# Optimization experiments

Hardware: AMD Instinct MI355X
Metric: run time of the kernel (lower is better)

The kernel has to match this reference:

```python
import jax, jax.numpy as jnp
import numpy as np

BN_EPS = 1e-5
STRIDE = 8  # encoder output stride -> upsample target is H*8


def conv2d(x, w, pad):
    return jax.lax.conv_general_dilated(
        x, w, (1, 1), [(pad, pad), (pad, pad)],
        dimension_numbers=('NCHW', 'OIHW', 'NCHW'))


def batchnorm(x, gamma, beta):
    # training-mode BN (batch statistics), matching a freshly-constructed torch module
    m = jnp.mean(x, axis=(0, 2, 3), keepdims=True)
    v = jnp.var(x, axis=(0, 2, 3), keepdims=True)
    xn = (x - m) * jax.lax.rsqrt(v + BN_EPS)
    return xn * gamma[None, :, None, None] + beta[None, :, None, None]


def setup_inputs() -> dict:
    key = jax.random.key(0)
    ks = jax.random.split(key, 8)
    B, C, H, W = 8, 256, 60, 60
    NC = 2
    return {
        'V_a': jax.random.normal(ks[0], (B, C, H, W), jnp.float32),
        'V_b': jax.random.normal(ks[1], (B, C, H, W), jnp.float32),
        'W_sim': jax.random.normal(ks[2], (C, C), jnp.float32) * 0.02,
        'gate_w': jax.random.normal(ks[3], (1, C, 1, 1), jnp.float32) * 0.01,
        'convA_w': jax.random.normal(ks[4], (C, 2 * C, 3, 3), jnp.float32) * 0.01,
        'convB_w': jax.random.normal(ks[5], (C, 2 * C, 3, 3), jnp.float32) * 0.01,
        'bnA_gamma': jnp.ones((C,), jnp.float32),
        'bnA_beta': jnp.zeros((C,), jnp.float32),
        'bnB_gamma': jnp.ones((C,), jnp.float32),
        'bnB_beta': jnp.zeros((C,), jnp.float32),
        'clsA_w': jax.random.normal(ks[6], (NC, C, 1, 1), jnp.float32) * 0.01,
        'clsA_b': jnp.zeros((NC,), jnp.float32),
        'clsB_w': jax.random.normal(ks[7], (NC, C, 1, 1), jnp.float32) * 0.01,
        'clsB_b': jnp.zeros((NC,), jnp.float32),
    }


def reference(V_a, V_b, W_sim, gate_w, convA_w, convB_w,
              bnA_gamma, bnA_beta, bnB_gamma, bnB_beta,
              clsA_w, clsA_b, clsB_w, clsB_b):
    B, C, H, W = V_a.shape
    HW = H * W
    out_h, out_w = H * STRIDE, W * STRIDE

    Va = V_a.reshape(B, C, HW)  # [B,C,HW_a]
    Vb = V_b.reshape(B, C, HW)  # [B,C,HW_b]

    # Linear on V_a^T: out[b,i,d] = sum_c Va[b,c,i] * W_sim[d,c]
    WVa = jnp.einsum('dc,bci->bdi', W_sim, Va)           # [B,C,HW_a]
    S = jnp.einsum('bdi,bdj->bij', WVa, Vb)              # [B,HW_a,HW_b]

    S_row = jax.nn.softmax(S, axis=1)                    # softmax over a-positions
    A_col = jax.nn.softmax(S, axis=2)                    # softmax over b-positions

    Z_b = jnp.einsum('bci,bij->bcj', Va, S_row).reshape(B, C, H, W)
    Z_a = jnp.einsum('bcj,bij->bci', Vb, A_col).reshape(B, C, H, W)

    mask_a = jax.nn.sigmoid(conv2d(Z_a, gate_w, 0))
    mask_b = jax.lax.stop_gradient(jax.nn.sigmoid(conv2d(Z_b, gate_w, 0)))
    Z_a = Z_a * mask_a
    Z_b = Z_b * mask_b

    Z_a = jnp.concatenate([Z_a, V_a], axis=1)            # [B,2C,H,W]
    Z_b = jnp.concatenate([Z_b, V_b], axis=1)

    Z_a = jax.nn.relu(batchnorm(conv2d(Z_a, convA_w, 1), bnA_gamma, bnA_beta))
    Z_b = jax.nn.relu(batchnorm(conv2d(Z_b, convB_w, 1), bnB_gamma, bnB_beta))

    x1 = conv2d(Z_a, clsA_w, 0) + clsA_b[None, :, None, None]
    x2 = conv2d(Z_b, clsB_w, 0) + clsB_b[None, :, None, None]

    NC = x1.shape[1]
    x1 = jax.image.resize(x1, (B, NC, out_h, out_w), method='bilinear')
    x2 = jax.image.resize(x2, (B, NC, out_h, out_w), method='bilinear')

    return jnp.stack([jax.nn.sigmoid(x1), jax.nn.sigmoid(x2)])  # [2,B,NC,out_h,out_w]
```

## Files before the change

### kernel.cpp

```cpp
#include <hip/hip_runtime.h>

#define C_CH   256
#define BATCH  8
#define HW     3600
#define CHW    (C_CH*HW)
#define NPIX   (BATCH*HW)
#define KCONV  4608
#define OHW    480
#define KP     3648
#define NROWP  3712
#define XPIX   3844
#define NT     57

typedef __attribute__((ext_vector_type(8))) short s16x8;
typedef __attribute__((ext_vector_type(4))) float f32x4;

__device__ __forceinline__ unsigned short f2bf(float f){
  unsigned int u = __float_as_uint(f);
  u += 0x7FFF + ((u>>16)&1);
  return (unsigned short)(u>>16);
}

__device__ __forceinline__ void gload16(const void* g, void* l){
  __builtin_amdgcn_global_load_lds((const __attribute__((address_space(1))) void*)g,
                                   (__attribute__((address_space(3))) void*)l, 16, 0, 0);
}

__device__ __forceinline__ void gemm_core(const char* a0, const char* b0,
                                          size_t lda, size_t ldb, int nkt,
                                          f32x4 acc[4][4]){
  __shared__ __align__(16) char LDS[32768];
  const int tid = threadIdx.x, l = tid & 63, w = tid >> 6;
  char* AsW = LDS + w*1024;
  char* BsW = LDS + 16384 + w*1024;
  const int arow = (w>>1)*64 + (l&15);
  const int brow = (w&1)*64 + (l&15);
  const int kc0 = (((l>>4)*16)      ) ^ ((l&7)<<4);
  const int kc1 = (((l>>4)*16) + 64 ) ^ ((l&7)<<4);
  const char* Ab = LDS;
  const char* Bb = LDS + 16384;
  for (int kt = 0; kt < nkt; ++kt){
#pragma unroll
    for (int i=0;i<4;i++){
      gload16(a0 + (size_t)(i*32)*lda + (size_t)kt*128, AsW + i*4096);
      gload16(b0 + (size_t)(i*32)*ldb + (size_t)kt*128, BsW + i*4096);
    }
    asm volatile("s_waitcnt vmcnt(0)" ::: "memory");
    __syncthreads();
    s16x8 af[4][2], bf[4][2];
#pragma unroll
    for (int f=0;f<4;f++){
      af[f][0] = *(const s16x8*)(Ab + (arow+f*16)*128 + kc0);
      af[f][1] = *(const s16x8*)(Ab + (arow+f*16)*128 + kc1);
      bf[f][0] = *(const s16x8*)(Bb + (brow+f*16)*128 + kc0);
      bf[f][1] = *(const s16x8*)(Bb + (brow+f*16)*128 + kc1);
    }
#pragma unroll
    for (int ks=0;ks<2;ks++)
#pragma unroll
      for (int fm=0;fm<4;fm++)
#pragma unroll
        for (int fn=0;fn<4;fn++)
          acc[fm][fn] = __builtin_amdgcn_mfma_f32_16x16x32_bf16(af[fm][ks], bf[fn][ks], acc[fm][fn], 0,0,0);
    __syncthreads();
  }
}

__global__ __launch_bounds__(256) void k_gemm_wva(const unsigned short* __restrict__ VaT,
                                                  const unsigned short* __restrict__ Wsim16,
                                                  unsigned short* __restrict__ WVaT){
  const int tid = threadIdx.x, l = tid&63, w = tid>>6;
  const int b = blockIdx.z;
  const int n0 = blockIdx.x*128, m0 = blockIdx.y*128;
  const int colS = ((tid&7)*16) ^ (((tid>>3)&7)<<4);
  const char* a0 = (const char*)(VaT + (size_t)b*NROWP*256) + (size_t)(m0 + (tid>>3))*512 + colS;
  const char* b0 = (const char*)Wsim16 + (size_t)(n0 + (tid>>3))*512 + colS;
  f32x4 acc[4][4] = {};
  gemm_core(a0, b0, 512, 512, 4, acc);
  unsigned short* ob = WVaT + (size_t)b*NROWP*256;
  const int mb = m0 + (w>>1)*64 + (l>>4)*4;
  const int nb = n0 + (w&1)*64 + (l&15);
#pragma unroll
  for (int fm=0;fm<4;fm++)
#pragma unroll
    for (int fn=0;fn<4;fn++){
      int n = nb + fn*16;
#pragma unroll
      for (int r=0;r<4;r++){
        int m = mb + fm*16 + r;
        if (m < HW) ob[(size_t)m*256 + n] = f2bf(acc[fm][fn][r]);
      }
    }
}

__global__ __launch_bounds__(256) void flash_attn(const char* __restrict__ WVaT,
                                                  const char* __restrict__ VbT,
                                                  const char* __restrict__ VaT,
                                                  const char* __restrict__ Va16,
                                                  const char* __restrict__ Vb16,
                                                  const float* __restrict__ gw,
                                                  unsigned short* __restrict__ XtA,
                                                  unsigned short* __restrict__ XtB){
  __shared__ __align__(16) char LDS[73728];
  const int tid = threadIdx.x, l = tid&63, w = tid>>6;
  const int b = blockIdx.y, side = blockIdx.z;
  const size_t tOff = (size_t)b*NROWP*512;
  const size_t vOff = (size_t)b*256*KP*2;
  const char* QT = (side ? VbT  : WVaT) + tOff;
  const char* Kt = (side ? WVaT : VbT ) + tOff;
  const char* Vp = (side ? Va16 : Vb16) + vOff;
  const char* Vc = (side ? VbT  : VaT ) + tOff;
  unsigned short* Xt = (side ? XtB : XtA) + (size_t)b*XPIX*512;
  const int i0 = blockIdx.x*64;

  char* Kls = LDS;
  char* Vls = LDS + 32768;
  char* Pls = LDS + 65536;

  s16x8 q[8];
  {
    const char* qp = QT + (size_t)(i0 + w*16 + (l&15))*512 + (l>>4)*16;
#pragma unroll
    for (int ks=0;ks<8;ks++) q[ks] = *(const s16x8*)(qp + ks*64);
  }
  float gwv[4];
#pragma unroll
  for (int fn=0;fn<4;fn++) gwv[fn] = gw[w*64 + fn*16 + (l&15)];

  f32x4 acc[4][4] = {};
  f32x4 lac = {0.f,0.f,0.f,0.f};

  auto stageK = [&](int t){
    const char* src = Kt + (size_t)t*32768;
#pragma unroll
    for (int p=0;p<8;p++){
      int row = p*8 + (tid>>5), ch = tid&31;
      gload16(src + (size_t)row*512 + ((ch*16) ^ ((row&7)<<4)), Kls + p*4096 + tid*16);
    }
  };
  auto stageV = [&](int t){
#pragma unroll
    for (int p=0;p<8;p++){
      int row = p*32 + (tid>>3), ch = tid&7;
      gload16(Vp + (size_t)row*(KP*2) + (size_t)t*128 + ((ch*16) ^ ((row&7)<<4)),
              Vls + p*4096 + tid*16);
    }
  };

  stageK(0); stageV(0);
  asm volatile("s_waitcnt vmcnt(0)" ::: "memory");
  __syncthreads();

  for (int t=0; t<NT; ++t){
    f32x4 sac[4] = {};
#pragma unroll
    for (int ks=0;ks<8;ks++){
      s16x8 bk[4];
#pragma unroll
      for (int fn=0;fn<4;fn++){
        int row = fn*16 + (l&15);
        bk[fn] = *(const s16x8*)(Kls + row*512 + ((ks*64 + (l>>4)*16) ^ ((row&7)<<4)));
      }
#pragma unroll
      for (int fn=0;fn<4;fn++)
        sac[fn] = __builtin_amdgcn_mfma_f32_16x16x32_bf16(q[ks], bk[fn], sac[fn], 0,0,0);
    }
    const int j0 = t*64;
#pragma unroll
    for (int fn=0;fn<4;fn++){
      int col = fn*16 + (l&15);
      bool jv = (j0 + col) < HW;
#pragma unroll
      for (int r=0;r<4;r++){
        float e = jv ? __expf(sac[fn][r]) : 0.f;
        lac[r] += e;
        int row = w*16 + (l>>4)*4 + r;
        *(unsigned short*)(Pls + row*128 + ((col*2) ^ ((row&7)<<4))) = f2bf(e);
      }
    }
    __syncthreads();
    if (t+1 < NT) stageK(t+1);
#pragma unroll
    for (int ks=0;ks<2;ks++){
      s16x8 ap[4], bv[4];
#pragma unroll
      for (int fm=0;fm<4;fm++){
        int row = fm*16 + (l&15);
        ap[fm] = *(const s16x8*)(Pls + row*128 + ((ks*64 + (l>>4)*16) ^ ((row&7)<<4)));
      }
#pragma unroll
      for (int fn=0;fn<4;fn++){
        int row = w*64 + fn*16 + (l&15);
        bv[fn] = *(const s16x8*)(Vls + row*128 + ((ks*64 + (l>>4)*16) ^ ((row&7)<<4)));
      }
#pragma unroll
      for (int fm=0;fm<4;fm++)
#pragma unroll
        for (int fn=0;fn<4;fn++)
          acc[fm][fn] = __builtin_amdgcn_mfma_f32_16x16x32_bf16(ap[fm], bv[fn], acc[fm][fn], 0,0,0);
    }
    __syncthreads();
    if (t+1 < NT){
      stageV(t+1);
      asm volatile("s_waitcnt vmcnt(0)" ::: "memory");
    }
    __syncthreads();
  }

  float* Lred = (float*)(LDS + 65536);
  float* Mls  = Lred + 64;
  float* Gp   = Mls + 64;
#pragma unroll
  for (int r=0;r<4;r++){
    float v = lac[r];
    v += __shfl_xor(v,1); v += __shfl_xor(v,2); v += __shfl_xor(v,4); v += __shfl_xor(v,8);
    if ((l&15)==0) Lred[w*16 + (l>>4)*4 + r] = 1.f / v;
  }
  __syncthreads();
#pragma unroll
  for (int fm=0;fm<4;fm++){
#pragma unroll
    for (int r=0;r<4;r++){
      float v = acc[fm][0][r]*gwv[0] + acc[fm][1][r]*gwv[1]
              + acc[fm][2][r]*gwv[2] + acc[fm][3][r]*gwv[3];
      v += __shfl_xor(v,1); v += __shfl_xor(v,2); v += __shfl_xor(v,4); v += __shfl_xor(v,8);
      if ((l&15)==0) Gp[w*64 + fm*16 + (l>>4)*4 + r] = v;
    }
  }
  __syncthreads();
  if (tid < 64){
    float g = (Gp[tid] + Gp[64+tid] + Gp[128+tid] + Gp[192+tid]) * Lred[tid];
    Mls[tid] = 1.f/(1.f + __expf(-g));
  }
  __syncthreads();
  char* Ost = LDS;
#pragma unroll
  for (int fm=0;fm<4;fm++){
    float4 li = *(const float4*)&Lred[fm*16 + (l>>4)*4];
    float4 mk = *(const float4*)&Mls [fm*16 + (l>>4)*4];
    float s0 = li.x*mk.x, s1 = li.y*mk.y, s2 = li.z*mk.z, s3 = li.w*mk.w;
#pragma unroll
    for (int fn=0;fn<4;fn++){
      int col = w*64 + fn*16 + (l&15);
      int row = fm*16 + (l>>4)*4;
      *(unsigned short*)(Ost + (row+0)*512 + col*2) = f2bf(acc[fm][fn][0]*s0);
      *(unsigned short*)(Ost + (row+1)*512 + col*2) = f2bf(acc[fm][fn][1]*s1);
      *(unsigned short*)(Ost + (row+2)*512 + col*2) = f2bf(acc[fm][fn][2]*s2);
      *(unsigned short*)(Ost + (row+3)*512 + col*2) = f2bf(acc[fm][fn][3]*s3);
    }
  }
  __syncthreads();
  {
    int row = tid>>2, ch = tid&3;
    int p = i0 + row;
    if (p < HW){
      int y = p/60, x = p - y*60;
      char* dst = (char*)Xt + (size_t)((y+1)*62 + (x+1))*1024 + ch*128;
      const char* osrc = Ost + row*512 + ch*128;
      const char* vsrc = Vc + (size_t)p*512 + ch*128;
#pragma unroll
      for (int q8=0;q8<8;q8++) *(uint4*)(dst + q8*16) = *(const uint4*)(osrc + q8*16);
#pragma unroll
      for (int q8=0;q8<8;q8++) *(uint4*)(dst + 512 + q8*16) = *(const uint4*)(vsrc + q8*16);
    }
  }
}

__global__ __launch_bounds__(256) void k_gemm_conv(const unsigned short* __restrict__ WcA,
                                                   const unsigned short* __restrict__ WcB,
                                                   const unsigned short* __restrict__ XtA,
                                                   const unsigned short* __restrict__ XtB,
                                                   float* __restrict__ Ra, float* __restrict__ Rb){
  __shared__ __align__(16) char LDS[32768];
  const int tid = threadIdx.x, l = tid&63, w = tid>>6;
  const unsigned short* Wc = blockIdx.z ? WcB : WcA;
  const unsigned short* Xt = blockIdx.z ? XtB : XtA;
  float* R = blockIdx.z ? Rb : Ra;
  const int n0 = blockIdx.x*128, m0 = blockIdx.y*128;
  const int colS = ((tid&7)*16) ^ (((tid>>3)&7)<<4);
  const int srow = tid>>3;
  const char* a0 = (const char*)Wc + (size_t)(m0+srow)*(KCONV*2) + colS;
  size_t bbase[4];
#pragma unroll
  for (int i=0;i<4;i++){
    int n = n0 + i*32 + srow;
    int bb = n/HW, p = n - bb*HW;
    int y = p/60, x = p - y*60;
    bbase[i] = ((size_t)bb*XPIX + (size_t)(y+1)*62 + (x+1))*1024 + colS;
  }
  char* AsW = LDS + w*1024;
  char* BsW = LDS + 16384 + w*1024;
  const int arow = (w>>1)*64 + (l&15);
  const int brow = (w&1)*64 + (l&15);
  const int kc0 = (((l>>4)*16)      ) ^ ((l&7)<<4);
  const int kc1 = (((l>>4)*16) + 64 ) ^ ((l&7)<<4);
  const char* Ab = LDS;
  const char* Bb = LDS + 16384;
  f32x4 acc[4][4] = {};
  for (int kt = 0; kt < 72; ++kt){
    const int sh = kt>>3;
    const int ci0b = (kt&7)*128;
    const int dy = sh/3 - 1, dx = (sh - (sh/3)*3) - 1;
    const int boff = (dy*62 + dx)*1024 + ci0b;
#pragma unroll
    for (int i=0;i<4;i++){
      gload16(a0 + (size_t)(i*32)*(KCONV*2) + (size_t)kt*128, AsW + i*4096);
      gload16((const char*)Xt + bbase[i] + boff, BsW + i*4096);
    }
    asm volatile("s_waitcnt vmcnt(0)" ::: "memory");
    __syncthreads();
    s16x8 af[4][2], bfr[4][2];
#pragma unroll
    for (int f=0;f<4;f++){
      af[f][0]  = *(const s16x8*)(Ab + (arow+f*16)*128 + kc0);
      af[f][1]  = *(const s16x8*)(Ab + (arow+f*16)*128 + kc1);
      bfr[f][0] = *(const s16x8*)(Bb + (brow+f*16)*128 + kc0);
      bfr[f][1] = *(const s16x8*)(Bb + (brow+f*16)*128 + kc1);
    }
#pragma unroll
    for (int ks=0;ks<2;ks++)
#pragma unroll
      for (int fm=0;fm<4;fm++)
#pragma unroll
        for (int fn=0;fn<4;fn++)
          acc[fm][fn] = __builtin_amdgcn_mfma_f32_16x16x32_bf16(af[fm][ks], bfr[fn][ks], acc[fm][fn], 0,0,0);
    __syncthreads();
  }
  const int mb = m0 + (w>>1)*64 + (l>>4)*4;
  const int nb = n0 + (w&1)*64 + (l&15);
#pragma unroll
  for (int fm=0;fm<4;fm++)
#pragma unroll
    for (int fn=0;fn<4;fn++){
      int n = nb + fn*16;
      int bb = n/HW, p = n - bb*HW;
      float* op = R + (size_t)bb*CHW + (size_t)(mb+fm*16)*HW + p;
#pragma unroll
      for (int r=0;r<4;r++) op[(size_t)r*HW] = acc[fm][fn][r];
    }
}

__global__ __launch_bounds__(256) void zerok(uint4* __restrict__ p, int n){
  int i = blockIdx.x*256 + threadIdx.x;
  if (i < n) p[i] = make_uint4(0,0,0,0);
}

__global__ __launch_bounds__(256) void convert_bf16(const float* __restrict__ in, unsigned short* __restrict__ out, int n){
  int i = blockIdx.x*256 + threadIdx.x;
  if (i < n) out[i] = f2bf(in[i]);
}

__global__ __launch_bounds__(256) void convw(const float* __restrict__ in, unsigned short* __restrict__ out){
  int idx = blockIdx.x*256 + threadIdx.x;
  int co = idx / KCONV;
  int kp = idx - co*KCONV;
  int sh = kp >> 9, ci = kp & 511;
  out[idx] = f2bf(in[co*KCONV + ci*9 + sh]);
}

__global__ __launch_bounds__(256) void convv(const float* __restrict__ in, unsigned short* __restrict__ out){
  int idx = blockIdx.x*256 + threadIdx.x;
  int row = idx / KP;
  int k = idx - row*KP;
  out[idx] = (k < HW) ? f2bf(in[(size_t)row*HW + k]) : 0;
}

__global__ __launch_bounds__(256) void convt(const float* __restrict__ in, unsigned short* __restrict__ out){
  __shared__ unsigned short T[64][66];
  const int b = blockIdx.y;
  const int i0 = blockIdx.x*64;
  const float* inb = in + (size_t)b*CHW;
  unsigned short* ob = out + (size_t)b*NROWP*256;
  for (int cc=0; cc<4; ++cc){
    __syncthreads();
    int i = i0 + (threadIdx.x & 63);
    int ic = i < HW ? i : HW-1;
#pragma unroll
    for (int r=0;r<16;r++){
      int cl = (threadIdx.x>>6)*16 + r;
      T[cl][threadIdx.x & 63] = f2bf(inb[(size_t)(cc*64+cl)*HW + ic]);
    }
    __syncthreads();
    int il = threadIdx.x>>2, seg = threadIdx.x&3;
    unsigned short tmp[16];
#pragma unroll
    for (int e=0;e<16;e++) tmp[e] = T[seg*16+e][il];
    *(s16x8*)(ob + (size_t)(i0+il)*256 + cc*64 + seg*16)     = *(const s16x8*)tmp;
    *(s16x8*)(ob + (size_t)(i0+il)*256 + cc*64 + seg*16 + 8) = *(const s16x8*)(tmp+8);
  }
}

__global__ __launch_bounds__(256) void bn_stats(const float* __restrict__ X, float* __restrict__ sums){
  int co = blockIdx.x;
  float s = 0.f, ss = 0.f;
  for (int i = threadIdx.x; i < NPIX; i += 256){
    int bi = i / HW, p = i - bi*HW;
    float v = X[(size_t)bi*CHW + (size_t)co*HW + p];
    s += v; ss += v*v;
  }
  __shared__ float rs[256], rss[256];
  rs[threadIdx.x] = s; rss[threadIdx.x] = ss; __syncthreads();
  for (int off=128; off>0; off>>=1){
    if (threadIdx.x < off){ rs[threadIdx.x] += rs[threadIdx.x+off]; rss[threadIdx.x] += rss[threadIdx.x+off]; }
    __syncthreads();
  }
  if (threadIdx.x==0){ sums[co] = rs[0]; sums[256+co] = rss[0]; }
}

__global__ __launch_bounds__(256) void cls_kernel(const float* __restrict__ R, const float* __restrict__ sums,
                                                  const float* __restrict__ gamma, const float* __restrict__ beta,
                                                  const float* __restrict__ cw, const float* __restrict__ cb,
                                                  float* __restrict__ Xout){
  __shared__ float red[2][4][64];
  int tx = threadIdx.x & 63, ty = threadIdx.x >> 6;
  int n = blockIdx.x*64 + tx;
  int bi = n / HW, p = n - bi*HW;
  float a0 = 0.f, a1 = 0.f;
  const float invN = 1.f/28800.f;
  for (int c = ty*64; c < ty*64+64; ++c){
    float mean = sums[c]*invN;
    float var  = sums[256+c]*invN - mean*mean;
    float sc   = gamma[c]*rsqrtf(var + 1e-5f);
    float shv  = beta[c] - mean*sc;
    float v = R[(size_t)bi*CHW + (size_t)c*HW + p]*sc + shv;
    v = fmaxf(v, 0.f);
    a0 += v*cw[c]; a1 += v*cw[256+c];
  }
  red[0][ty][tx] = a0; red[1][ty][tx] = a1; __syncthreads();
  if (ty==0){
    float r0 = red[0][0][tx]+red[0][1][tx]+red[0][2][tx]+red[0][3][tx] + cb[0];
    float r1 = red[1][0][tx]+red[1][1][tx]+red[1][2][tx]+red[1][3][tx] + cb[1];
    Xout[((size_t)bi*2 + 0)*HW + p] = r0;
    Xout[((size_t)bi*2 + 1)*HW + p] = r1;
  }
}

__global__ __launch_bounds__(256) void resize_kernel(const float* __restrict__ X1, const float* __restrict__ X2,
                                                     float* __restrict__ Out){
  int idx = blockIdx.x*256 + threadIdx.x;
  int ox = idx % OHW; int t = idx / OHW;
  int oy = t % OHW;  t /= OHW;
  int nc = t & 1;    t >>= 1;
  int bi = t & 7;    int s = t >> 3;
  const float* X = (s == 0) ? X1 : X2;
  float fy = (oy + 0.5f)*0.125f - 0.5f;
  float fx = (ox + 0.5f)*0.125f - 0.5f;
  float y0f = floorf(fy), x0f = floorf(fx);
  float wy = fy - y0f, wx = fx - x0f;
  int y0 = (int)y0f, x0 = (int)x0f;
  int y1 = min(max(y0+1,0),59), x1 = min(max(x0+1,0),59);
  y0 = min(max(y0,0),59); x0 = min(max(x0,0),59);
  const float* Xp = X + ((size_t)bi*2 + nc)*HW;
  float v00 = Xp[y0*60+x0], v01 = Xp[y0*60+x1];
  float v10 = Xp[y1*60+x0], v11 = Xp[y1*60+x1];
  float v = v00*(1.f-wy)*(1.f-wx) + v01*(1.f-wy)*wx + v10*wy*(1.f-wx) + v11*wy*wx;
  Out[idx] = 1.f/(1.f+__expf(-v));
}

extern "C" void kernel_launch(void* const* d_in, const int* in_sizes, int n_in,
                              void* d_out, int out_size, void* d_ws, size_t ws_size,
                              hipStream_t stream){
  const float* Va    = (const float*)d_in[0];
  const float* Vb    = (const float*)d_in[1];
  const float* Wsim  = (const float*)d_in[2];
  const float* gw    = (const float*)d_in[3];
  const float* cwA   = (const float*)d_in[4];
  const float* cwB   = (const float*)d_in[5];
  const float* gA    = (const float*)d_in[6];
  const float* bA    = (const float*)d_in[7];
  const float* gB    = (const float*)d_in[8];
  const float* bB    = (const float*)d_in[9];
  const float* clsAw = (const float*)d_in[10];
  const float* clsAb = (const float*)d_in[11];
  const float* clsBw = (const float*)d_in[12];
  const float* clsBb = (const float*)d_in[13];
  float* out = (float*)d_out;

  char* wsb = (char*)d_ws;
  size_t off = 0;
  auto alloc = [&](size_t bytes)->void*{
    void* pt = wsb + off;
    off += (bytes + 255) & ~(size_t)255;
    return pt;
  };
  unsigned short* Va16   = (unsigned short*)alloc((size_t)8*256*KP*2);
  unsigned short* Vb16   = (unsigned short*)alloc((size_t)8*256*KP*2);
  unsigned short* VaT16  = (unsigned short*)alloc((size_t)8*NROWP*256*2);
  unsigned short* VbT16  = (unsigned short*)alloc((size_t)8*NROWP*256*2);
  unsigned short* WVaT16 = (unsigned short*)alloc((size_t)8*NROWP*256*2);
  unsigned short* Wsim16 = (unsigned short*)alloc((size_t)256*256*2);
  unsigned short* WcA16  = (unsigned short*)alloc((size_t)256*KCONV*2);
  unsigned short* WcB16  = (unsigned short*)alloc((size_t)256*KCONV*2);
  unsigned short* XtA    = (unsigned short*)alloc((size_t)8*XPIX*512*2);
  unsigned short* XtB    = (unsigned short*)alloc((size_t)8*XPIX*512*2);
  float* sumsA= (float*)alloc(512*4);
  float* sumsB= (float*)alloc(512*4);
  float* Ra = (float*)Va16;
  float* Rb = (float*)VaT16;
  float* x1 = (float*)WVaT16;
  float* x2 = x1 + (size_t)BATCH*2*HW;

  zerok<<<dim3(15376), dim3(256), 0, stream>>>((uint4*)XtA, 3936256);
  convert_bf16<<<dim3(256), dim3(256), 0, stream>>>(Wsim, Wsim16, 65536);
  convw<<<dim3(4608), dim3(256), 0, stream>>>(cwA, WcA16);
  convw<<<dim3(4608), dim3(256), 0, stream>>>(cwB, WcB16);
  convv<<<dim3(29184), dim3(256), 0, stream>>>(Va, Va16);
  convv<<<dim3(29184), dim3(256), 0, stream>>>(Vb, Vb16);
  convt<<<dim3(57,8), dim3(256), 0, stream>>>(Va, VaT16);
  convt<<<dim3(57,8), dim3(256), 0, stream>>>(Vb, VbT16);
  k_gemm_wva<<<dim3(2,29,8), dim3(256), 0, stream>>>(VaT16, Wsim16, WVaT16);

  flash_attn<<<dim3(57,8,2), dim3(256), 0, stream>>>(
      (const char*)WVaT16, (const char*)VbT16, (const char*)VaT16,
      (const char*)Va16, (const char*)Vb16, gw, XtA, XtB);

  k_gemm_conv<<<dim3(225,2,2), dim3(256), 0, stream>>>(WcA16, WcB16, XtA, XtB, Ra, Rb);
  bn_stats<<<dim3(256), dim3(256), 0, stream>>>(Ra, sumsA);
  bn_stats<<<dim3(256), dim3(256), 0, stream>>>(Rb, sumsB);
  cls_kernel<<<dim3(450), dim3(256), 0, stream>>>(Ra, sumsA, gA, bA, clsAw, clsAb, x1);
  cls_kernel<<<dim3(450), dim3(256), 0, stream>>>(Rb, sumsB, gB, bB, clsBw, clsBb, x2);
  resize_kernel<<<dim3(28800), dim3(256), 0, stream>>>(x1, x2, out);
}
```

Measured before the change: 852.8 us.

## Load V tiles directly into registers and shrink LDS for higher occupancy

Removes the LDS staging buffer for the V operand in the flash attention kernel, so each wave loads its V fragments straight from global memory into registers at the top of each tile iteration. This cuts LDS from 72KB to 40KB, drops one pair of barriers per iteration, and adds a launch-bounds hint for three blocks per CU. The P-tile swizzle changes to match the new layout. In exchange, V reads are uncoalesced per-lane 16-byte global loads with higher latency exposure, and there is extra register pressure from holding bv.

```diff
diff --git a/kernel.cpp b/kernel.cpp
--- a/kernel.cpp
+++ b/kernel.cpp
@@ -93,7 +93,7 @@
     }
 }
 
-__global__ __launch_bounds__(256) void flash_attn(const char* __restrict__ WVaT,
+__global__ __launch_bounds__(256, 3) void flash_attn(const char* __restrict__ WVaT,
                                                   const char* __restrict__ VbT,
                                                   const char* __restrict__ VaT,
                                                   const char* __restrict__ Va16,
@@ -101,7 +101,7 @@
                                                   const float* __restrict__ gw,
                                                   unsigned short* __restrict__ XtA,
                                                   unsigned short* __restrict__ XtB){
-  __shared__ __align__(16) char LDS[73728];
+  __shared__ __align__(16) char LDS[40960];
   const int tid = threadIdx.x, l = tid&63, w = tid>>6;
   const int b = blockIdx.y, side = blockIdx.z;
   const size_t tOff = (size_t)b*NROWP*512;
@@ -114,8 +114,7 @@
   const int i0 = blockIdx.x*64;
 
   char* Kls = LDS;
-  char* Vls = LDS + 32768;
-  char* Pls = LDS + 65536;
+  char* Pls = LDS + 32768;
 
   s16x8 q[8];
   {
@@ -138,20 +137,21 @@
       gload16(src + (size_t)row*512 + ((ch*16) ^ ((row&7)<<4)), Kls + p*4096 + tid*16);
     }
   };
-  auto stageV = [&](int t){
-#pragma unroll
-    for (int p=0;p<8;p++){
-      int row = p*32 + (tid>>3), ch = tid&7;
-      gload16(Vp + (size_t)row*(KP*2) + (size_t)t*128 + ((ch*16) ^ ((row&7)<<4)),
-              Vls + p*4096 + tid*16);
-    }
-  };
-
-  stageK(0); stageV(0);
+
+  stageK(0);
   asm volatile("s_waitcnt vmcnt(0)" ::: "memory");
   __syncthreads();
 
+  const char* vrow = Vp + (size_t)(w*64 + (l&15))*(KP*2) + (l>>4)*16;
+  const int g = l>>4;
+
   for (int t=0; t<NT; ++t){
+    s16x8 bv[2][4];
+#pragma unroll
+    for (int ks=0;ks<2;ks++)
+#pragma unroll
+      for (int fn=0;fn<4;fn++)
+        bv[ks][fn] = *(const s16x8*)(vrow + (size_t)fn*16*(KP*2) + (size_t)t*128 + ks*64);
     f32x4 sac[4] = {};
 #pragma unroll
     for (int ks=0;ks<8;ks++){
@@ -174,40 +174,31 @@
       for (int r=0;r<4;r++){
         float e = jv ? __expf(sac[fn][r]) : 0.f;
         lac[r] += e;
-        int row = w*16 + (l>>4)*4 + r;
-        *(unsigned short*)(Pls + row*128 + ((col*2) ^ ((row&7)<<4))) = f2bf(e);
+        int row = w*16 + g*4 + r;
+        *(unsigned short*)(Pls + row*128 + ((col*2) ^ (g<<5))) = f2bf(e);
       }
     }
     __syncthreads();
     if (t+1 < NT) stageK(t+1);
 #pragma unroll
     for (int ks=0;ks<2;ks++){
-      s16x8 ap[4], bv[4];
+      s16x8 ap[4];
 #pragma unroll
       for (int fm=0;fm<4;fm++){
         int row = fm*16 + (l&15);
-        ap[fm] = *(const s16x8*)(Pls + row*128 + ((ks*64 + (l>>4)*16) ^ ((row&7)<<4)));
+        ap[fm] = *(const s16x8*)(Pls + row*128 + ((ks*64 + (l>>4)*16) ^ ((((l&15)>>2)&3)<<5)));
       }
 #pragma unroll
-      for (int fn=0;fn<4;fn++){
-        int row = w*64 + fn*16 + (l&15);
-        bv[fn] = *(const s16x8*)(Vls + row*128 + ((ks*64 + (l>>4)*16) ^ ((row&7)<<4)));
-      }
-#pragma unroll
       for (int fm=0;fm<4;fm++)
 #pragma unroll
         for (int fn=0;fn<4;fn++)
-          acc[fm][fn] = __builtin_amdgcn_mfma_f32_16x16x32_bf16(ap[fm], bv[fn], acc[fm][fn], 0,0,0);
-    }
-    __syncthreads();
-    if (t+1 < NT){
-      stageV(t+1);
-      asm volatile("s_waitcnt vmcnt(0)" ::: "memory");
-    }
-    __syncthreads();
-  }
-
-  float* Lred = (float*)(LDS + 65536);
+          acc[fm][fn] = __builtin_amdgcn_mfma_f32_16x16x32_bf16(ap[fm], bv[ks][fn], acc[fm][fn], 0,0,0);
+    }
+    asm volatile("s_waitcnt vmcnt(0)" ::: "memory");
+    __syncthreads();
+  }
+
+  float* Lred = (float*)(LDS + 32768);
   float* Mls  = Lred + 64;
   float* Gp   = Mls + 64;
 #pragma unroll
@@ -229,8 +220,8 @@
   }
   __syncthreads();
   if (tid < 64){
-    float g = (Gp[tid] + Gp[64+tid] + Gp[128+tid] + Gp[192+tid]) * Lred[tid];
-    Mls[tid] = 1.f/(1.f + __expf(-g));
+    float gt = (Gp[tid] + Gp[64+tid] + Gp[128+tid] + Gp[192+tid]) * Lred[tid];
+    Mls[tid] = 1.f/(1.f + __expf(-gt));
   }
   __syncthreads();
   char* Ost = LDS;
```

New measurement: 1.046 ms. 1.23x slower.
